# Kernel optimization log

Hardware: AMD Instinct MI355X
Metric: run time of the kernel (lower is better)

Reference implementation:

```python
import jax, jax.numpy as jnp
import numpy as np

H = 8            # num_heads
HID = 128        # hidden_channels
D = HID // H     # per-head dim
L = 2            # num_layers
NCLS = 4         # out_channels (number of 1-class heads)


def _forward(x_a, x_b, lin_W_a, lin_b_a, lin_W_b, lin_b_b,
             Wk, bk, Wq, bq, Wv, bv, arel, mrel, prel,
             Wa, ba_out, skip, Wcls, bcls, edges):
    """HGT forward. edges: list of (src_type, dst_type, [2,E] int array); list
    position is the relation index into arel/mrel/prel."""
    # per-type input projection + ReLU
    x = [jax.nn.relu(x_a @ lin_W_a + lin_b_a),
         jax.nn.relu(x_b @ lin_W_b + lin_b_b)]
    N = [x[0].shape[0], x[1].shape[0]]
    scale = 1.0 / np.sqrt(D)
    for l in range(L):
        # per-type K/Q/V projections -> [N, H, D]
        k = [(x[t] @ Wk[l, t] + bk[l, t]).reshape(N[t], H, D) for t in range(2)]
        q = [(x[t] @ Wq[l, t] + bq[l, t]).reshape(N[t], H, D) for t in range(2)]
        v = [(x[t] @ Wv[l, t] + bv[l, t]).reshape(N[t], H, D) for t in range(2)]
        new_x = []
        for dt in range(2):
            logits, vals, dsts = [], [], []
            for r, (s_t, d_t, ei) in enumerate(edges):
                if d_t != dt:
                    continue
                src, dst = ei[0], ei[1]
                # relation-specific per-head transforms of gathered src K/V
                ke = jnp.einsum('ehd,hdf->ehf', k[s_t][src], arel[l, r])  # [E,H,D]
                ve = jnp.einsum('ehd,hdf->ehf', v[s_t][src], mrel[l, r])  # [E,H,D]
                a = jnp.sum(q[dt][dst] * ke, axis=-1) * prel[l, r] * scale  # [E,H]
                logits.append(a); vals.append(ve); dsts.append(dst)
            a = jnp.concatenate(logits, axis=0)
            ve = jnp.concatenate(vals, axis=0)
            dst = jnp.concatenate(dsts, axis=0)
            # segment softmax over all incoming edges per destination node
            amax = jax.ops.segment_max(a, dst, num_segments=N[dt])           # [N,H]
            ae = jnp.exp(a - amax[dst])                                       # [E,H]
            den = jax.ops.segment_sum(ae, dst, num_segments=N[dt])           # [N,H]
            msg = jax.ops.segment_sum(ae[:, :, None] * ve, dst,
                                      num_segments=N[dt])                    # [N,H,D]
            out = (msg / jnp.maximum(den, 1e-16)[:, :, None]).reshape(N[dt], HID)
            # output projection with GELU + learned skip gate
            out = jax.nn.gelu(out) @ Wa[l, dt] + ba_out[l, dt]
            beta = jax.nn.sigmoid(skip[l, dt])
            new_x.append(beta * out + (1.0 - beta) * x[dt])
        x = new_x
    # node_to_predict == 'a'; concatenated 1-class heads -> [Na, NCLS]
    return x[0] @ Wcls.T + bcls


def setup_inputs() -> dict:
    key = jax.random.key(0)
    ks = iter(jax.random.split(key, 40))
    Na, Nb, E = 50000, 50000, 150000
    def rn(shape, fan_in):
        return jax.random.normal(next(ks), shape, dtype=jnp.float32) / np.sqrt(fan_in)
    inp = {
        'x_a': jax.random.normal(next(ks), (Na, 64), dtype=jnp.float32),
        'x_b': jax.random.normal(next(ks), (Nb, 32), dtype=jnp.float32),
        'lin_W_a': rn((64, HID), 64), 'lin_b_a': jnp.zeros((HID,), jnp.float32),
        'lin_W_b': rn((32, HID), 32), 'lin_b_b': jnp.zeros((HID,), jnp.float32),
        'Wk': rn((L, 2, HID, HID), HID), 'bk': jnp.zeros((L, 2, HID), jnp.float32),
        'Wq': rn((L, 2, HID, HID), HID), 'bq': jnp.zeros((L, 2, HID), jnp.float32),
        'Wv': rn((L, 2, HID, HID), HID), 'bv': jnp.zeros((L, 2, HID), jnp.float32),
        'arel': rn((L, 4, H, D, D), D), 'mrel': rn((L, 4, H, D, D), D),
        'prel': jnp.ones((L, 4, H), jnp.float32),
        'Wa': rn((L, 2, HID, HID), HID), 'ba_out': jnp.zeros((L, 2, HID), jnp.float32),
        'skip': jnp.ones((L, 2), jnp.float32),
        'Wcls': rn((NCLS, HID), HID), 'bcls': jnp.zeros((NCLS,), jnp.float32),
        'edge_aa': jax.random.randint(next(ks), (2, E), 0, Na, dtype=jnp.int32),
        'edge_ab': jax.random.randint(next(ks), (2, E), 0, Na, dtype=jnp.int32),
        'edge_ba': jax.random.randint(next(ks), (2, E), 0, Na, dtype=jnp.int32),
        'edge_bb': jax.random.randint(next(ks), (2, E), 0, Nb, dtype=jnp.int32),
    }
    return inp


def reference(x_a, x_b, lin_W_a, lin_b_a, lin_W_b, lin_b_b,
              Wk, bk, Wq, bq, Wv, bv, arel, mrel, prel,
              Wa, ba_out, skip, Wcls, bcls,
              edge_aa, edge_ab, edge_ba, edge_bb):
    edges = [(0, 0, edge_aa), (0, 1, edge_ab), (1, 0, edge_ba), (1, 1, edge_bb)]
    return _forward(x_a, x_b, lin_W_a, lin_b_a, lin_W_b, lin_b_b,
                    Wk, bk, Wq, bq, Wv, bv, arel, mrel, prel,
                    Wa, ba_out, skip, Wcls, bcls, edges)
```

## Files before the change

kernel.cpp:

```cpp
#include <hip/hip_runtime.h>
#include <math.h>

#define HIDC 128
#define NH 8
#define HD 16
#define NCLS 4

typedef __attribute__((ext_vector_type(8))) short s8v;
typedef __attribute__((ext_vector_type(4))) float f4v;

#define ST_STRIDE 264
#define ST_BYTES  (64 * ST_STRIDE * 2)

__device__ __forceinline__ float gelu_f(float h) {
    float z = 0.7978845608028654f * (h + 0.044715f * h * h * h);
    float t = 1.f - 2.f / (1.f + __expf(2.f * z));
    return 0.5f * h * (1.f + t);
}
__device__ __forceinline__ unsigned short f2bf(float x) {
    unsigned b = __float_as_uint(x);
    unsigned r = (b + 0x7FFFu + ((b >> 16) & 1u)) >> 16;
    return (unsigned short)r;
}
__device__ __forceinline__ float bf2f(unsigned short u) {
    return __uint_as_float(((unsigned)u) << 16);
}
__device__ __forceinline__ void gload_lds16(const void* g, void* l) {
    __builtin_amdgcn_global_load_lds(
        (const __attribute__((address_space(1))) unsigned int*)g,
        (__attribute__((address_space(3))) unsigned int*)l, 16, 0, 0);
}

__global__ void zero_u32(unsigned* __restrict__ p, long n)
{
    long i = (long)blockIdx.x * blockDim.x + threadIdx.x;
    long stride = (long)gridDim.x * blockDim.x;
    for (; i < n; i += stride) p[i] = 0u;
}

__global__ void fold_all(const float* __restrict__ Wk, const float* __restrict__ bk,
                         const float* __restrict__ Wv, const float* __restrict__ bv,
                         const float* __restrict__ arel, const float* __restrict__ mrel,
                         float* __restrict__ Wt, float* __restrict__ bt)
{
    __shared__ float rsh[NH * HD * HD];
    int bid = blockIdx.x;
    int w = bid & 1, r = (bid >> 1) & 3, l = bid >> 3;
    int st = r >> 1;
    const float* W   = (w ? Wv : Wk) + (size_t)(l * 2 + st) * HIDC * HIDC;
    const float* bb  = (w ? bv : bk) + (size_t)(l * 2 + st) * HIDC;
    const float* rel = (w ? mrel : arel) + (size_t)(l * 4 + r) * NH * HD * HD;
    float* wt  = Wt + (size_t)bid * HIDC * HIDC;
    float* btp = bt + (size_t)bid * HIDC;

    int t = threadIdx.x;
    for (int i = t; i < NH * HD * HD; i += 128) rsh[i] = rel[i];
    __syncthreads();
    int h = t >> 4, f = t & 15;
    const float* rh = rsh + h * HD * HD + f;
    for (int k = 0; k < HIDC; ++k) {
        float acc = 0.f;
        const float* wr = W + (size_t)k * HIDC + h * HD;
        #pragma unroll
        for (int d = 0; d < HD; ++d) acc = fmaf(wr[d], rh[d * HD], acc);
        wt[(size_t)k * HIDC + t] = acc;
    }
    float accb = 0.f;
    const float* br = bb + h * HD;
    #pragma unroll
    for (int d = 0; d < HD; ++d) accb = fmaf(br[d], rh[d * HD], accb);
    btp[t] = accb;
}

__global__ __launch_bounds__(128)
void wsplit(const float* __restrict__ linWa, const float* __restrict__ linWb,
            const float* __restrict__ Wq, const float* __restrict__ Wa,
            const float* __restrict__ Wt, unsigned short* __restrict__ W2,
            int Ka, int Kb)
{
    int bid = blockIdx.x;
    int nka = Ka >> 5, nkb = Kb >> 5;
    const float* src; size_t moff; int ks, Km;
    if (bid < nka) { src = linWa; moff = 0; ks = bid; Km = Ka; }
    else if (bid < nka + nkb) { src = linWb; moff = (size_t)2 * Ka * 128; ks = bid - nka; Km = Kb; }
    else {
        int cc = bid - nka - nkb;
        int mm = cc >> 2; ks = cc & 3; Km = 128;
        moff = (size_t)2 * (Ka + Kb) * 128 + (size_t)mm * 32768;
        if (mm < 16)      src = Wt + (size_t)mm * 16384;
        else if (mm < 20) src = Wq + (size_t)(mm - 16) * 16384;
        else              src = Wa + (size_t)(mm - 20) * 16384;
    }
    int t = threadIdx.x;
    int fn = t >> 4, lr = t & 15;
    for (int g = 0; g < 4; ++g)
        for (int j = 0; j < 8; ++j) {
            int k = ks * 32 + g * 8 + j;
            float x = src[(size_t)k * 128 + fn * 16 + lr];
            unsigned short h = f2bf(x);
            size_t co = moff + (size_t)ks * 4096 + fn * 512 + g * 128 + lr * 8 + j;
            W2[co] = h;
            W2[co + (size_t)Km * 128] = f2bf(x - bf2f(h));
        }
}

__global__ void hist4(const int* __restrict__ d0, int E0, const int* __restrict__ d1, int E1,
                      const int* __restrict__ d2, int E2, const int* __restrict__ d3, int E3,
                      unsigned* __restrict__ cnt, int Nmax)
{
    int i = blockIdx.x * blockDim.x + threadIdx.x;
    int tot = E0 + E1 + E2 + E3;
    int stride = gridDim.x * blockDim.x;
    for (; i < tot; i += stride) {
        int j = i; const int* p; int dt;
        if (j < E0) { p = d0; dt = 0; }
        else { j -= E0;
            if (j < E1) { p = d1; dt = 1; }
            else { j -= E1;
                if (j < E2) { p = d2; dt = 0; }
                else { j -= E2; p = d3; dt = 1; }
            }
        }
        atomicAdd(&cnt[(size_t)dt * Nmax + p[j]], 1u);
    }
}

__global__ __launch_bounds__(256)
void scan_p1(const unsigned* __restrict__ cnt, unsigned* __restrict__ bsum,
             int Nmax, int nblk, int n0, int n1)
{
    int ty = blockIdx.x / nblk, b = blockIdx.x % nblk;
    int n = ty ? n1 : n0;
    const unsigned* c = cnt + (size_t)ty * Nmax;
    int i0 = b * 1024 + threadIdx.x * 4;
    unsigned s = 0;
    #pragma unroll
    for (int j = 0; j < 4; ++j) { int i = i0 + j; if (i < n) s += c[i]; }
    __shared__ unsigned sh[256];
    sh[threadIdx.x] = s; __syncthreads();
    for (int off = 128; off; off >>= 1) {
        if (threadIdx.x < (unsigned)off) sh[threadIdx.x] += sh[threadIdx.x + off];
        __syncthreads();
    }
    if (threadIdx.x == 0) bsum[blockIdx.x] = sh[0];
}

__global__ __launch_bounds__(256)
void scan_p2(unsigned* __restrict__ bsum, int nblk, int* __restrict__ rowptr,
             int Nmax, int n0, int n1)
{
    __shared__ unsigned sh[256];
    int tot = 2 * nblk;
    int t = threadIdx.x;
    unsigned v = (t < tot) ? bsum[t] : 0u;
    sh[t] = v; __syncthreads();
    for (int off = 1; off < 256; off <<= 1) {
        unsigned add = (t >= off) ? sh[t - off] : 0u;
        __syncthreads(); sh[t] += add; __syncthreads();
    }
    unsigned t0 = sh[nblk - 1];
    unsigned tall = sh[255];
    unsigned excl = sh[t] - v;
    if (t < tot) bsum[t] = (t < nblk) ? excl : excl - t0;
    if (t == 0) {
        rowptr[n0] = (int)t0;
        rowptr[(Nmax + 1) + n1] = (int)(tall - t0);
    }
}

__global__ __launch_bounds__(256)
void scan_p3(const unsigned* __restrict__ cnt, const unsigned* __restrict__ bsum,
             int* __restrict__ rowptr, unsigned* __restrict__ cursor,
             int Nmax, int nblk, int n0, int n1)
{
    int ty = blockIdx.x / nblk, b = blockIdx.x % nblk;
    int n = ty ? n1 : n0;
    const unsigned* c = cnt + (size_t)ty * Nmax;
    int* rp = rowptr + (size_t)ty * (Nmax + 1);
    unsigned* cur = cursor + (size_t)ty * Nmax;
    int t = threadIdx.x;
    int i0 = b * 1024 + t * 4;
    unsigned v[4]; unsigned s = 0;
    #pragma unroll
    for (int j = 0; j < 4; ++j) { int i = i0 + j; v[j] = (i < n) ? c[i] : 0u; s += v[j]; }
    __shared__ unsigned sh[256];
    sh[t] = s; __syncthreads();
    for (int off = 1; off < 256; off <<= 1) {
        unsigned add = (t >= off) ? sh[t - off] : 0u;
        __syncthreads(); sh[t] += add; __syncthreads();
    }
    unsigned run = bsum[blockIdx.x] + sh[t] - s;
    #pragma unroll
    for (int j = 0; j < 4; ++j) {
        int i = i0 + j;
        if (i < n) { rp[i] = (int)run; cur[i] = run; }
        run += v[j];
    }
}

__global__ void scatter4(const int* __restrict__ e0, int E0, const int* __restrict__ e1, int E1,
                         const int* __restrict__ e2, int E2, const int* __restrict__ e3, int E3,
                         unsigned* __restrict__ cursor, int Nmax,
                         unsigned* __restrict__ adj0, unsigned* __restrict__ adj1)
{
    int i = blockIdx.x * blockDim.x + threadIdx.x;
    int tot = E0 + E1 + E2 + E3;
    int stride = gridDim.x * blockDim.x;
    for (; i < tot; i += stride) {
        int j = i; const int* e; int E; int dt; unsigned rb;
        if (j < E0) { e = e0; E = E0; dt = 0; rb = 0u; }
        else { j -= E0;
            if (j < E1) { e = e1; E = E1; dt = 1; rb = 0u; }
            else { j -= E1;
                if (j < E2) { e = e2; E = E2; dt = 0; rb = 1u << 24; }
                else { j -= E2; e = e3; E = E3; dt = 1; rb = 1u << 24; }
            }
        }
        int s = e[j], d = e[E + j];
        unsigned pos = atomicAdd(&cursor[(size_t)dt * Nmax + d], 1u);
        (dt ? adj1 : adj0)[pos] = (unsigned)s | rb;
    }
}

template <int ASPLIT, int EPI, int OUT, int NK>
__global__ __launch_bounds__(256)
void mg2p(const void* __restrict__ Ain, const unsigned short* __restrict__ Whi,
          const float* __restrict__ bias,
          const unsigned short* __restrict__ xold, const float* __restrict__ skipp,
          void* __restrict__ Cout, int N)
{
    constexpr int K = NK * 32;
    constexpr int PB = NK * 8192;
    constexpr size_t LSZ = (OUT == 2 && ST_BYTES > PB) ? ST_BYTES : PB;
    __shared__ char ldsraw[LSZ];
    unsigned short* lds = (unsigned short*)ldsraw;
    int t = threadIdx.x;
    constexpr int NCP = PB / (16 * 256);
    #pragma unroll
    for (int i = 0; i < NCP; ++i)
        gload_lds16((const char*)Whi + ((size_t)t + i * 256) * 16,
                    ldsraw + ((size_t)t + i * 256) * 16);
    __syncthreads();

    int w = t >> 6, lane = t & 63;
    int lr = lane & 15, g = lane >> 4;
    int row0 = blockIdx.x * 64;
    int fnb = w * 2;

    f4v acc[4][2];
    #pragma unroll
    for (int i = 0; i < 4; ++i) { acc[i][0] = (f4v)0.f; acc[i][1] = (f4v)0.f; }

    #pragma unroll
    for (int ks = 0; ks < NK; ++ks) {
        s8v ah[4], al[4];
        #pragma unroll
        for (int fm = 0; fm < 4; ++fm) {
            int row = row0 + fm * 16 + lr;
            if (row < N) {
                if (ASPLIT) {
                    const unsigned short* ap = (const unsigned short*)Ain + (size_t)row * 256 + ks * 32 + g * 8;
                    ah[fm] = *(const s8v*)ap;
                    al[fm] = *(const s8v*)(ap + 128);
                } else {
                    const float* ap = (const float*)Ain + (size_t)row * K + ks * 32 + g * 8;
                    float4 p = *(const float4*)ap;
                    float4 q = *(const float4*)(ap + 4);
                    float xv[8] = {p.x, p.y, p.z, p.w, q.x, q.y, q.z, q.w};
                    #pragma unroll
                    for (int j = 0; j < 8; ++j) {
                        unsigned short h = f2bf(xv[j]);
                        ah[fm][j] = (short)h;
                        al[fm][j] = (short)f2bf(xv[j] - bf2f(h));
                    }
                }
            } else { ah[fm] = (s8v)0; al[fm] = (s8v)0; }
        }
        #pragma unroll
        for (int f = 0; f < 2; ++f) {
            size_t co = (size_t)ks * 8192 + (fnb + f) * 1024 + g * 256 + lr * 16;
            s8v b = *(const s8v*)(ldsraw + co);
            #pragma unroll
            for (int fm = 0; fm < 4; ++fm) {
                acc[fm][f] = __builtin_amdgcn_mfma_f32_16x16x32_bf16(ah[fm], b, acc[fm][f], 0, 0, 0);
                acc[fm][f] = __builtin_amdgcn_mfma_f32_16x16x32_bf16(al[fm], b, acc[fm][f], 0, 0, 0);
            }
        }
    }

    float beta = 0.f;
    if (EPI == 2) beta = 1.f / (1.f + __expf(-skipp[0]));
    int rb = g * 4;

    if (OUT == 2) {
        __syncthreads();
        #pragma unroll
        for (int f = 0; f < 2; ++f) {
            int col = (fnb + f) * 16 + lr;
            float bv = bias[col];
            #pragma unroll
            for (int fm = 0; fm < 4; ++fm) {
                #pragma unroll
                for (int j = 0; j < 4; ++j) {
                    int lrow = fm * 16 + rb + j;
                    int row = row0 + lrow;
                    float o = acc[fm][f][j] + bv;
                    if (EPI == 1) o = fmaxf(o, 0.f);
                    if (EPI == 2) {
                        float xo = (row < N) ? (bf2f(xold[(size_t)row * 256 + col]) +
                                                bf2f(xold[(size_t)row * 256 + 128 + col])) : 0.f;
                        o = beta * o + (1.f - beta) * xo;
                    }
                    unsigned short h = f2bf(o);
                    lds[(size_t)lrow * ST_STRIDE + col] = h;
                    lds[(size_t)lrow * ST_STRIDE + 128 + col] = f2bf(o - bf2f(h));
                }
            }
        }
        __syncthreads();
        unsigned short* C = (unsigned short*)Cout;
        #pragma unroll
        for (int it = 0; it < 8; ++it) {
            int d4 = (it * 256 + t) * 4;
            int row = d4 >> 7, c2 = d4 & 127;
            int grow = row0 + row;
            if (grow < N) {
                uint4 v = *(const uint4*)(lds + (size_t)row * ST_STRIDE + c2 * 2);
                *(uint4*)(C + (size_t)grow * 256 + c2 * 2) = v;
            }
        }
    } else {
        float* C = (float*)Cout;
        #pragma unroll
        for (int f = 0; f < 2; ++f) {
            int col = (fnb + f) * 16 + lr;
            float bv = bias[col];
            #pragma unroll
            for (int fm = 0; fm < 4; ++fm) {
                #pragma unroll
                for (int j = 0; j < 4; ++j) {
                    int row = row0 + fm * 16 + rb + j;
                    if (row < N) C[(size_t)row * HIDC + col] = acc[fm][f][j] + bv;
                }
            }
        }
    }
}

struct KvArgs {
    const unsigned short* A[4];
    const unsigned short* Wm[4];
    const float* bias[4];
    unsigned short* out[4];
    int N[4];
    int cum[5];
};

__global__ __launch_bounds__(256)
void mgemm_kv4(KvArgs args)
{
    int bid = blockIdx.x;
    int jb = 0;
    while (jb < 3 && bid >= args.cum[jb + 1]) ++jb;
    int lb = bid - args.cum[jb];
    const unsigned short* Ain = args.A[jb];
    const unsigned short* Wkt = args.Wm[jb];
    const unsigned short* Wvt = args.Wm[jb] + 32768;
    const float* bias2 = args.bias[jb];
    unsigned short* kv = args.out[jb];
    int N = args.N[jb];

    __shared__ char ldsraw[65536];
    unsigned short* lds = (unsigned short*)ldsraw;
    int t = threadIdx.x;
    #pragma unroll
    for (int i = 0; i < 8; ++i)
        gload_lds16((const char*)Wkt + ((size_t)t + i * 256) * 16,
                    ldsraw + ((size_t)t + i * 256) * 16);
    #pragma unroll
    for (int i = 0; i < 8; ++i)
        gload_lds16((const char*)Wvt + ((size_t)t + i * 256) * 16,
                    ldsraw + 32768 + ((size_t)t + i * 256) * 16);

    int w = t >> 6, lane = t & 63;
    int lr = lane & 15, g = lane >> 4;
    int row0 = lb * 64;
    int fnb = w * 2;

    s8v ah[4][4], al[4][4];
    #pragma unroll
    for (int fm = 0; fm < 4; ++fm) {
        int row = row0 + fm * 16 + lr;
        #pragma unroll
        for (int ks = 0; ks < 4; ++ks) {
            if (row < N) {
                const unsigned short* ap = Ain + (size_t)row * 256 + ks * 32 + g * 8;
                ah[fm][ks] = *(const s8v*)ap;
                al[fm][ks] = *(const s8v*)(ap + 128);
            } else { ah[fm][ks] = (s8v)0; al[fm][ks] = (s8v)0; }
        }
    }
    __syncthreads();

    f4v acck[4][2], accv[4][2];
    #pragma unroll
    for (int i = 0; i < 4; ++i) {
        acck[i][0] = (f4v)0.f; acck[i][1] = (f4v)0.f;
        accv[i][0] = (f4v)0.f; accv[i][1] = (f4v)0.f;
    }

    #pragma unroll
    for (int ks = 0; ks < 4; ++ks) {
        #pragma unroll
        for (int f = 0; f < 2; ++f) {
            int fn = fnb + f;
            size_t co = (size_t)ks * 8192 + fn * 1024 + g * 256 + lr * 16;
            s8v bk_ = *(const s8v*)(ldsraw + co);
            s8v bv_ = *(const s8v*)(ldsraw + 32768 + co);
            #pragma unroll
            for (int fm = 0; fm < 4; ++fm) {
                acck[fm][f] = __builtin_amdgcn_mfma_f32_16x16x32_bf16(ah[fm][ks], bk_, acck[fm][f], 0, 0, 0);
                acck[fm][f] = __builtin_amdgcn_mfma_f32_16x16x32_bf16(al[fm][ks], bk_, acck[fm][f], 0, 0, 0);
                accv[fm][f] = __builtin_amdgcn_mfma_f32_16x16x32_bf16(ah[fm][ks], bv_, accv[fm][f], 0, 0, 0);
                accv[fm][f] = __builtin_amdgcn_mfma_f32_16x16x32_bf16(al[fm][ks], bv_, accv[fm][f], 0, 0, 0);
            }
        }
    }

    __syncthreads();
    int rb = g * 4;
    #pragma unroll
    for (int f = 0; f < 2; ++f) {
        int fn = fnb + f;
        int col = fn * 16 + lr;
        float bk0 = bias2[col], bv0 = bias2[128 + col];
        #pragma unroll
        for (int fm = 0; fm < 4; ++fm) {
            #pragma unroll
            for (int j = 0; j < 4; ++j) {
                int lrow = fm * 16 + rb + j;
                lds[(size_t)lrow * ST_STRIDE + col] = f2bf(acck[fm][f][j] + bk0);
                lds[(size_t)lrow * ST_STRIDE + 128 + col] = f2bf(accv[fm][f][j] + bv0);
            }
        }
    }
    __syncthreads();
    #pragma unroll
    for (int it = 0; it < 8; ++it) {
        int d4 = (it * 256 + t) * 4;
        int row = d4 >> 7, c2 = d4 & 127;
        int grow = row0 + row;
        if (grow < N) {
            uint4 v = *(const uint4*)(lds + (size_t)row * ST_STRIDE + c2 * 2);
            *(uint4*)(kv + (size_t)grow * 256 + c2 * 2) = v;
        }
    }
}

#define EDGE_STEP(IDX, M, S, AX, AY)                                               \
    {                                                                              \
        unsigned ent = adj[IDX];                                                   \
        int src = (int)(ent & 0xFFFFFFu);                                          \
        const unsigned short* kv = (ent >> 24) ? kvB : kvA;                        \
        float sp = (ent >> 24) ? spB : spA;                                        \
        ushort2 kraw = *(const ushort2*)(kv + (size_t)src * 256 + lane * 2);       \
        ushort2 vraw = *(const ushort2*)(kv + (size_t)src * 256 + 128 + lane * 2); \
        float p = bf2f(kraw.x) * qv.x + bf2f(kraw.y) * qv.y;                       \
        p += __shfl_xor(p, 1, 8);                                                  \
        p += __shfl_xor(p, 2, 8);                                                  \
        p += __shfl_xor(p, 4, 8);                                                  \
        float a = p * sp;                                                          \
        float mn = fmaxf(M, a);                                                    \
        float cc = __expf(M - mn);                                                 \
        float pe = __expf(a - mn);                                                 \
        S = S * cc + pe;                                                           \
        AX = AX * cc + pe * bf2f(vraw.x);                                          \
        AY = AY * cc + pe * bf2f(vraw.y);                                          \
        M = mn;                                                                    \
    }

__global__ __launch_bounds__(256)
void agg_fused(const float* __restrict__ Q,
               const unsigned short* __restrict__ kvA, const unsigned short* __restrict__ kvB,
               const int* __restrict__ rowptr, const unsigned* __restrict__ adj,
               const float* __restrict__ prelA, const float* __restrict__ prelB,
               float scale, unsigned short* __restrict__ msgs, int N)
{
    int node = blockIdx.x * 4 + (threadIdx.x >> 6);
    if (node >= N) return;
    int lane = threadIdx.x & 63;
    int h = lane >> 3;
    float spA = prelA[h] * scale, spB = prelB[h] * scale;
    float2 qv = *(const float2*)(Q + (size_t)node * HIDC + lane * 2);
    int beg = rowptr[node], end = rowptr[node + 1];

    float m0 = -INFINITY, s0 = 0.f, ax0 = 0.f, ay0 = 0.f;
    float m1 = -INFINITY, s1 = 0.f, ax1 = 0.f, ay1 = 0.f;
    int i = beg;
    for (; i + 1 < end; i += 2) {
        EDGE_STEP(i,     m0, s0, ax0, ay0);
        EDGE_STEP(i + 1, m1, s1, ax1, ay1);
    }
    if (i < end) EDGE_STEP(i, m0, s0, ax0, ay0);

    float ox = 0.f, oy = 0.f;
    if (end > beg) {
        float mn = fmaxf(m0, m1);
        float c0 = __expf(m0 - mn), c1 = __expf(m1 - mn);
        float s = s0 * c0 + s1 * c1;
        float inv = 1.f / fmaxf(s, 1e-16f);
        ox = (ax0 * c0 + ax1 * c1) * inv;
        oy = (ay0 * c0 + ay1 * c1) * inv;
    }
    ox = gelu_f(ox); oy = gelu_f(oy);
    unsigned short hx = f2bf(ox), hy = f2bf(oy);
    size_t base = (size_t)node * 256 + lane * 2;
    ushort2 hi2; hi2.x = hx; hi2.y = hy;
    ushort2 lo2; lo2.x = f2bf(ox - bf2f(hx)); lo2.y = f2bf(oy - bf2f(hy));
    *(ushort2*)(msgs + base) = hi2;
    *(ushort2*)(msgs + base + 128) = lo2;
}

__global__ __launch_bounds__(256)
void cls_kernel(const unsigned short* __restrict__ X, const float* __restrict__ Wc,
                const float* __restrict__ bc, float* __restrict__ out, int N)
{
    int row = blockIdx.x * 4 + (threadIdx.x >> 6);
    if (row >= N) return;
    int lane = threadIdx.x & 63;
    const unsigned short* xr = X + (size_t)row * 256 + lane * 2;
    float x0 = bf2f(xr[0]) + bf2f(xr[128]);
    float x1 = bf2f(xr[1]) + bf2f(xr[129]);
    float p0, p1, p2, p3;
    {
        float2 w0 = *(const float2*)(Wc + 0 * HIDC + lane * 2);
        float2 w1 = *(const float2*)(Wc + 1 * HIDC + lane * 2);
        float2 w2 = *(const float2*)(Wc + 2 * HIDC + lane * 2);
        float2 w3 = *(const float2*)(Wc + 3 * HIDC + lane * 2);
        p0 = x0 * w0.x + x1 * w0.y;
        p1 = x0 * w1.x + x1 * w1.y;
        p2 = x0 * w2.x + x1 * w2.y;
        p3 = x0 * w3.x + x1 * w3.y;
    }
    #pragma unroll
    for (int off = 32; off; off >>= 1) {
        p0 += __shfl_xor(p0, off);
        p1 += __shfl_xor(p1, off);
        p2 += __shfl_xor(p2, off);
        p3 += __shfl_xor(p3, off);
    }
    if (lane < 4) {
        float v = (lane == 0) ? p0 : (lane == 1) ? p1 : (lane == 2) ? p2 : p3;
        out[(size_t)row * NCLS + lane] = v + bc[lane];
    }
}

extern "C" void kernel_launch(void* const* d_in, const int* in_sizes, int n_in,
                              void* d_out, int out_size, void* d_ws, size_t ws_size,
                              hipStream_t stream)
{
    const float* x_a    = (const float*)d_in[0];
    const float* x_b    = (const float*)d_in[1];
    const float* lin_W_a= (const float*)d_in[2];
    const float* lin_b_a= (const float*)d_in[3];
    const float* lin_W_b= (const float*)d_in[4];
    const float* lin_b_b= (const float*)d_in[5];
    const float* Wk     = (const float*)d_in[6];
    const float* bk     = (const float*)d_in[7];
    const float* Wq     = (const float*)d_in[8];
    const float* bq     = (const float*)d_in[9];
    const float* Wv     = (const float*)d_in[10];
    const float* bv     = (const float*)d_in[11];
    const float* arel   = (const float*)d_in[12];
    const float* mrel   = (const float*)d_in[13];
    const float* prel   = (const float*)d_in[14];
    const float* Wa     = (const float*)d_in[15];
    const float* ba     = (const float*)d_in[16];
    const float* skip   = (const float*)d_in[17];
    const float* Wcls   = (const float*)d_in[18];
    const float* bcls   = (const float*)d_in[19];
    const int* eptr[4] = {(const int*)d_in[20], (const int*)d_in[21],
                          (const int*)d_in[22], (const int*)d_in[23]};
    int Ee[4] = {in_sizes[20] / 2, in_sizes[21] / 2, in_sizes[22] / 2, in_sizes[23] / 2};

    int Ka = in_sizes[2] / HIDC;
    int Kb = in_sizes[4] / HIDC;
    int Na = in_sizes[0] / Ka;
    int Nb = in_sizes[1] / Kb;
    int Nn[2] = {Na, Nb};
    int Nmax = Na > Nb ? Na : Nb;

    char* base = (char*)d_ws;
    unsigned short* xs[2];
    xs[0] = (unsigned short*)base; base += (size_t)Na * 256 * 2;
    xs[1] = (unsigned short*)base; base += (size_t)Nb * 256 * 2;
    float* qb[2];
    qb[0] = (float*)base; base += (size_t)Na * HIDC * 4;
    qb[1] = (float*)base; base += (size_t)Nb * HIDC * 4;
    unsigned short* kvb[2][2];
    for (int s = 0; s < 2; ++s)
        for (int d = 0; d < 2; ++d) { kvb[s][d] = (unsigned short*)base; base += (size_t)Nn[s] * 256 * 2; }
    unsigned short* msgs = (unsigned short*)base; base += (size_t)Nmax * 256 * 2;
    float* Wt = (float*)base; base += (size_t)16 * HIDC * HIDC * 4;
    float* bt = (float*)base; base += (size_t)16 * HIDC * 4;
    size_t nW2 = (size_t)2 * (Ka + Kb) * 128 + (size_t)24 * 32768;
    unsigned short* W2 = (unsigned short*)base; base += nW2 * 2;
    unsigned* cnt = (unsigned*)base; base += (size_t)2 * Nmax * 4;
    unsigned* cursor = (unsigned*)base; base += (size_t)2 * Nmax * 4;
    unsigned* bsum = (unsigned*)base; base += 256 * 4;
    int* rowptr = (int*)base; base += (size_t)2 * (Nmax + 1) * 4;
    unsigned* adj0 = (unsigned*)base; base += (size_t)(Ee[0] + Ee[2]) * 4;
    unsigned* adj1 = (unsigned*)base; base += (size_t)(Ee[1] + Ee[3]) * 4;

    size_t off_lina = 0;
    size_t off_linb = (size_t)2 * Ka * 128;
    size_t base128  = (size_t)2 * (Ka + Kb) * 128;
    auto offKT = [&](int l, int st, int dt) { return base128 + (size_t)(l * 8 + (st * 2 + dt) * 2) * 32768; };
    auto offQ  = [&](int l, int tt) { return base128 + (size_t)(16 + l * 2 + tt) * 32768; };
    auto offA  = [&](int l, int tt) { return base128 + (size_t)(20 + l * 2 + tt) * 32768; };

    fold_all<<<16, 128, 0, stream>>>(Wk, bk, Wv, bv, arel, mrel, Wt, bt);
    int nwblk = (Ka >> 5) + (Kb >> 5) + 24 * 4;
    wsplit<<<nwblk, 128, 0, stream>>>(lin_W_a, lin_W_b, Wq, Wa, Wt, W2, Ka, Kb);

    int nblk = (Nmax + 1023) / 1024;
    zero_u32<<<512, 256, 0, stream>>>(cnt, (long)2 * Nmax);
    hist4<<<1024, 256, 0, stream>>>(eptr[0] + Ee[0], Ee[0], eptr[1] + Ee[1], Ee[1],
                                    eptr[2] + Ee[2], Ee[2], eptr[3] + Ee[3], Ee[3],
                                    cnt, Nmax);
    scan_p1<<<2 * nblk, 256, 0, stream>>>(cnt, bsum, Nmax, nblk, Na, Nb);
    scan_p2<<<1, 256, 0, stream>>>(bsum, nblk, rowptr, Nmax, Na, Nb);
    scan_p3<<<2 * nblk, 256, 0, stream>>>(cnt, bsum, rowptr, cursor, Nmax, nblk, Na, Nb);
    scatter4<<<1024, 256, 0, stream>>>(eptr[0], Ee[0], eptr[1], Ee[1],
                                       eptr[2], Ee[2], eptr[3], Ee[3],
                                       cursor, Nmax, adj0, adj1);

    int gn64[2] = {(Na + 63) / 64, (Nb + 63) / 64};
    mg2p<0, 1, 2, 2><<<gn64[0], 256, 0, stream>>>(x_a, W2 + off_lina, lin_b_a,
                                                  nullptr, nullptr, xs[0], Na);
    mg2p<0, 1, 2, 1><<<gn64[1], 256, 0, stream>>>(x_b, W2 + off_linb, lin_b_b,
                                                  nullptr, nullptr, xs[1], Nb);

    const float scale = 0.25f;

    for (int l = 0; l < 2; ++l) {
        KvArgs ka;
        int cum = 0;
        for (int j = 0; j < 4; ++j) {
            int st = j >> 1, dt = j & 1;
            int bid = l * 8 + (st * 2 + dt) * 2;
            ka.A[j] = xs[st];
            ka.Wm[j] = W2 + offKT(l, st, dt);
            ka.bias[j] = bt + (size_t)bid * HIDC;
            ka.out[j] = kvb[st][dt];
            ka.N[j] = Nn[st];
            ka.cum[j] = cum;
            cum += gn64[st];
        }
        ka.cum[4] = cum;
        mgemm_kv4<<<cum, 256, 0, stream>>>(ka);

        mg2p<1, 0, 0, 4><<<gn64[1], 256, 0, stream>>>(xs[1], W2 + offQ(l, 1),
                                                      bq + (l * 2 + 1) * HIDC,
                                                      nullptr, nullptr, qb[1], Nn[1]);
        mg2p<1, 0, 0, 4><<<gn64[0], 256, 0, stream>>>(xs[0], W2 + offQ(l, 0),
                                                      bq + (l * 2 + 0) * HIDC,
                                                      nullptr, nullptr, qb[0], Nn[0]);

        agg_fused<<<(Nn[1] + 3) / 4, 256, 0, stream>>>(qb[1], kvb[0][1], kvb[1][1],
                                                       rowptr + (Nmax + 1), adj1,
                                                       prel + (l * 4 + 1) * NH, prel + (l * 4 + 3) * NH,
                                                       scale, msgs, Nn[1]);
        mg2p<1, 2, 2, 4><<<gn64[1], 256, 0, stream>>>(msgs, W2 + offA(l, 1),
                                                      ba + (l * 2 + 1) * HIDC,
                                                      xs[1], skip + (l * 2 + 1), xs[1], Nn[1]);
        agg_fused<<<(Nn[0] + 3) / 4, 256, 0, stream>>>(qb[0], kvb[0][0], kvb[1][0],
                                                       rowptr, adj0,
                                                       prel + (l * 4 + 0) * NH, prel + (l * 4 + 2) * NH,
                                                       scale, msgs, Nn[0]);
        mg2p<1, 2, 2, 4><<<gn64[0], 256, 0, stream>>>(msgs, W2 + offA(l, 0),
                                                      ba + (l * 2 + 0) * HIDC,
                                                      xs[0], skip + (l * 2 + 0), xs[0], Nn[0]);
    }

    cls_kernel<<<(Na + 3) / 4, 256, 0, stream>>>(xs[0], Wcls, bcls, (float*)d_out, Na);
}
```

Before: 623.0 us.

## Merge K, V and Q projection GEMMs into one ten-job grouped launch

Replaces the fused K+V kernel and the two separate Q projection launches with a single grouped GEMM kernel that has ten jobs: K and V halves are split into separate jobs, and Q jobs write float output. This cuts two kernel launches per layer and doubles the block count for the K/V work, while reducing per-block LDS and register use to raise occupancy. In exchange, each input row tile is now loaded twice, once for the K job and once for the V job, instead of being shared.

```diff
diff --git a/kernel.cpp b/kernel.cpp
--- a/kernel.cpp
+++ b/kernel.cpp
@@ -347,112 +347,126 @@
     }
 }
 
-struct KvArgs {
-    const unsigned short* A[4];
-    const unsigned short* Wm[4];
-    const float* bias[4];
-    unsigned short* out[4];
-    int N[4];
-    int cum[5];
+struct GJob {
+    const unsigned short* A;
+    const unsigned short* W;
+    const float* bias;
+    void* out;
+    int N;
+    int mode;
 };
+struct GArgs { GJob job[10]; int cum[11]; };
+
+#define Q_STRIDE 132
 
 __global__ __launch_bounds__(256)
-void mgemm_kv4(KvArgs args)
+void gemm10(GArgs args)
 {
     int bid = blockIdx.x;
     int jb = 0;
-    while (jb < 3 && bid >= args.cum[jb + 1]) ++jb;
+    while (jb < 9 && bid >= args.cum[jb + 1]) ++jb;
+    GJob J = args.job[jb];
     int lb = bid - args.cum[jb];
-    const unsigned short* Ain = args.A[jb];
-    const unsigned short* Wkt = args.Wm[jb];
-    const unsigned short* Wvt = args.Wm[jb] + 32768;
-    const float* bias2 = args.bias[jb];
-    unsigned short* kv = args.out[jb];
-    int N = args.N[jb];
-
-    __shared__ char ldsraw[65536];
+
+    __shared__ char ldsraw[ST_BYTES];
     unsigned short* lds = (unsigned short*)ldsraw;
+    float* ldsf = (float*)ldsraw;
     int t = threadIdx.x;
     #pragma unroll
     for (int i = 0; i < 8; ++i)
-        gload_lds16((const char*)Wkt + ((size_t)t + i * 256) * 16,
+        gload_lds16((const char*)J.W + ((size_t)t + i * 256) * 16,
                     ldsraw + ((size_t)t + i * 256) * 16);
-    #pragma unroll
-    for (int i = 0; i < 8; ++i)
-        gload_lds16((const char*)Wvt + ((size_t)t + i * 256) * 16,
-                    ldsraw + 32768 + ((size_t)t + i * 256) * 16);
+    __syncthreads();
 
     int w = t >> 6, lane = t & 63;
     int lr = lane & 15, g = lane >> 4;
     int row0 = lb * 64;
     int fnb = w * 2;
-
-    s8v ah[4][4], al[4][4];
-    #pragma unroll
-    for (int fm = 0; fm < 4; ++fm) {
-        int row = row0 + fm * 16 + lr;
-        #pragma unroll
-        for (int ks = 0; ks < 4; ++ks) {
+    int N = J.N;
+
+    f4v acc[4][2];
+    #pragma unroll
+    for (int i = 0; i < 4; ++i) { acc[i][0] = (f4v)0.f; acc[i][1] = (f4v)0.f; }
+
+    #pragma unroll
+    for (int ks = 0; ks < 4; ++ks) {
+        s8v ah[4], al[4];
+        #pragma unroll
+        for (int fm = 0; fm < 4; ++fm) {
+            int row = row0 + fm * 16 + lr;
             if (row < N) {
-                const unsigned short* ap = Ain + (size_t)row * 256 + ks * 32 + g * 8;
-                ah[fm][ks] = *(const s8v*)ap;
-                al[fm][ks] = *(const s8v*)(ap + 128);
-            } else { ah[fm][ks] = (s8v)0; al[fm][ks] = (s8v)0; }
-        }
-    }
-    __syncthreads();
-
-    f4v acck[4][2], accv[4][2];
-    #pragma unroll
-    for (int i = 0; i < 4; ++i) {
-        acck[i][0] = (f4v)0.f; acck[i][1] = (f4v)0.f;
-        accv[i][0] = (f4v)0.f; accv[i][1] = (f4v)0.f;
-    }
-
-    #pragma unroll
-    for (int ks = 0; ks < 4; ++ks) {
+                const unsigned short* ap = J.A + (size_t)row * 256 + ks * 32 + g * 8;
+                ah[fm] = *(const s8v*)ap;
+                al[fm] = *(const s8v*)(ap + 128);
+            } else { ah[fm] = (s8v)0; al[fm] = (s8v)0; }
+        }
         #pragma unroll
         for (int f = 0; f < 2; ++f) {
-            int fn = fnb + f;
-            size_t co = (size_t)ks * 8192 + fn * 1024 + g * 256 + lr * 16;
-            s8v bk_ = *(const s8v*)(ldsraw + co);
-            s8v bv_ = *(const s8v*)(ldsraw + 32768 + co);
+            size_t co = (size_t)ks * 8192 + (fnb + f) * 1024 + g * 256 + lr * 16;
+            s8v b = *(const s8v*)(ldsraw + co);
             #pragma unroll
             for (int fm = 0; fm < 4; ++fm) {
-                acck[fm][f] = __builtin_amdgcn_mfma_f32_16x16x32_bf16(ah[fm][ks], bk_, acck[fm][f], 0, 0, 0);
-                acck[fm][f] = __builtin_amdgcn_mfma_f32_16x16x32_bf16(al[fm][ks], bk_, acck[fm][f], 0, 0, 0);
-                accv[fm][f] = __builtin_amdgcn_mfma_f32_16x16x32_bf16(ah[fm][ks], bv_, accv[fm][f], 0, 0, 0);
-                accv[fm][f] = __builtin_amdgcn_mfma_f32_16x16x32_bf16(al[fm][ks], bv_, accv[fm][f], 0, 0, 0);
+                acc[fm][f] = __builtin_amdgcn_mfma_f32_16x16x32_bf16(ah[fm], b, acc[fm][f], 0, 0, 0);
+                acc[fm][f] = __builtin_amdgcn_mfma_f32_16x16x32_bf16(al[fm], b, acc[fm][f], 0, 0, 0);
             }
         }
     }
 
     __syncthreads();
     int rb = g * 4;
-    #pragma unroll
-    for (int f = 0; f < 2; ++f) {
-        int fn = fnb + f;
-        int col = fn * 16 + lr;
-        float bk0 = bias2[col], bv0 = bias2[128 + col];
-        #pragma unroll
-        for (int fm = 0; fm < 4; ++fm) {
+
+    if (J.mode < 2) {
+        #pragma unroll
+        for (int f = 0; f < 2; ++f) {
+            int col = (fnb + f) * 16 + lr;
+            float bv = J.bias[col];
             #pragma unroll
-            for (int j = 0; j < 4; ++j) {
-                int lrow = fm * 16 + rb + j;
-                lds[(size_t)lrow * ST_STRIDE + col] = f2bf(acck[fm][f][j] + bk0);
-                lds[(size_t)lrow * ST_STRIDE + 128 + col] = f2bf(accv[fm][f][j] + bv0);
-            }
-        }
-    }
-    __syncthreads();
-    #pragma unroll
-    for (int it = 0; it < 8; ++it) {
-        int d4 = (it * 256 + t) * 4;
-        int row = d4 >> 7, c2 = d4 & 127;
-        int grow = row0 + row;
-        if (grow < N) {
-            uint4 v = *(const uint4*)(lds + (size_t)row * ST_STRIDE + c2 * 2);
-            *(uint4*)(kv + (size_t)grow * 256 + c2 * 2) = v;
+            for (int fm = 0; fm < 4; ++fm) {
+                #pragma unroll
+                for (int j = 0; j < 4; ++j) {
+                    int lrow = fm * 16 + rb + j;
+                    lds[(size_t)lrow * 136 + col] = f2bf(acc[fm][f][j] + bv);
+                }
+            }
+        }
+        __syncthreads();
+        unsigned short* C = (unsigned short*)J.out;
+        int koff = J.mode * 128;
+        #pragma unroll
+        for (int it = 0; it < 4; ++it) {
+            int idx = it * 256 + t;
+            int row = idx >> 4, u = idx & 15;
+            int grow = row0 + row;
+            if (grow < N) {
+                uint4 v = *(const uint4*)(lds + (size_t)row * 136 + u * 8);
+                *(uint4*)(C + (size_t)grow * 256 + koff + u * 8) = v;
+            }
+        }
+    } else {
+        #pragma unroll
+        for (int f = 0; f < 2; ++f) {
+            int col = (fnb + f) * 16 + lr;
+            float bv = J.bias[col];
+            #pragma unroll
+            for (int fm = 0; fm < 4; ++fm) {
+                #pragma unroll
+                for (int j = 0; j < 4; ++j) {
+                    int lrow = fm * 16 + rb + j;
+                    ldsf[(size_t)lrow * Q_STRIDE + col] = acc[fm][f][j] + bv;
+                }
+            }
+        }
+        __syncthreads();
+        float* C = (float*)J.out;
+        #pragma unroll
+        for (int it = 0; it < 8; ++it) {
+            int idx = it * 256 + t;
+            int row = idx >> 5, u = idx & 31;
+            int grow = row0 + row;
+            if (grow < N) {
+                uint4 v = *(const uint4*)(ldsf + (size_t)row * Q_STRIDE + u * 4);
+                *(uint4*)(C + (size_t)grow * HIDC + u * 4) = v;
+            }
         }
     }
 }
@@ -644,28 +658,44 @@
     const float scale = 0.25f;
 
     for (int l = 0; l < 2; ++l) {
-        KvArgs ka;
+        GArgs ga;
         int cum = 0;
         for (int j = 0; j < 4; ++j) {
             int st = j >> 1, dt = j & 1;
             int bid = l * 8 + (st * 2 + dt) * 2;
-            ka.A[j] = xs[st];
-            ka.Wm[j] = W2 + offKT(l, st, dt);
-            ka.bias[j] = bt + (size_t)bid * HIDC;
-            ka.out[j] = kvb[st][dt];
-            ka.N[j] = Nn[st];
-            ka.cum[j] = cum;
+            ga.job[j].A = xs[st];
+            ga.job[j].W = W2 + offKT(l, st, dt);
+            ga.job[j].bias = bt + (size_t)bid * HIDC;
+            ga.job[j].out = kvb[st][dt];
+            ga.job[j].N = Nn[st];
+            ga.job[j].mode = 0;
+            ga.cum[j] = cum;
             cum += gn64[st];
         }
-        ka.cum[4] = cum;
-        mgemm_kv4<<<cum, 256, 0, stream>>>(ka);
-
-        mg2p<1, 0, 0, 4><<<gn64[1], 256, 0, stream>>>(xs[1], W2 + offQ(l, 1),
-                                                      bq + (l * 2 + 1) * HIDC,
-                                                      nullptr, nullptr, qb[1], Nn[1]);
-        mg2p<1, 0, 0, 4><<<gn64[0], 256, 0, stream>>>(xs[0], W2 + offQ(l, 0),
-                                                      bq + (l * 2 + 0) * HIDC,
-                                                      nullptr, nullptr, qb[0], Nn[0]);
+        for (int j = 0; j < 4; ++j) {
+            int st = j >> 1, dt = j & 1;
+            int bid = l * 8 + (st * 2 + dt) * 2;
+            ga.job[4 + j].A = xs[st];
+            ga.job[4 + j].W = W2 + offKT(l, st, dt) + 32768;
+            ga.job[4 + j].bias = bt + (size_t)(bid + 1) * HIDC;
+            ga.job[4 + j].out = kvb[st][dt];
+            ga.job[4 + j].N = Nn[st];
+            ga.job[4 + j].mode = 1;
+            ga.cum[4 + j] = cum;
+            cum += gn64[st];
+        }
+        for (int j = 0; j < 2; ++j) {
+            ga.job[8 + j].A = xs[j];
+            ga.job[8 + j].W = W2 + offQ(l, j);
+            ga.job[8 + j].bias = bq + (l * 2 + j) * HIDC;
+            ga.job[8 + j].out = qb[j];
+            ga.job[8 + j].N = Nn[j];
+            ga.job[8 + j].mode = 2;
+            ga.cum[8 + j] = cum;
+            cum += gn64[j];
+        }
+        ga.cum[10] = cum;
+        gemm10<<<cum, 256, 0, stream>>>(ga);
 
         agg_fused<<<(Nn[1] + 3) / 4, 256, 0, stream>>>(qb[1], kvb[0][1], kvb[1][1],
                                                        rowptr + (Nmax + 1), adj1,
```

New measurement: 664.2 us. +6.6%, slower.
